# Kernel tuning notes

Hardware: AMD Instinct MI355X
Metric: run time of the kernel (lower is better)

Reference implementation:

```python
import jax, jax.numpy as jnp
import numpy as np

V, E, H, T = 30000, 512, 512, 32
B, L = 64, 512


def setup_inputs() -> dict:
    key = jax.random.key(0)
    ks = jax.random.split(key, 14)
    n = lambda k, shape: (jax.random.normal(k, shape, jnp.float32) * 0.05)
    return {
        "x": jax.random.randint(ks[0], (B, L), 0, V),
        "embedding": n(ks[1], (V, E)),
        # PyTorch LSTM params, gate order (i, f, g, o); biases b_ih+b_hh fused
        "w_ih_f": n(ks[2], (4 * H, E)),
        "w_hh_f": n(ks[3], (4 * H, H)),
        "b_f": n(ks[4], (4 * H,)),
        "w_ih_b": n(ks[5], (4 * H, E)),
        "w_hh_b": n(ks[6], (4 * H, H)),
        "b_b": n(ks[7], (4 * H,)),
        "W": n(ks[8], (T, 2 * H)),
        "b": n(ks[9], (T,)),
        # CRF params (torchcrf)
        "start": n(ks[10], (T,)),
        "end": n(ks[11], (T,)),
        "trans": n(ks[12], (T, T)),
    }


def _lstm(x, w_ih, w_hh, bias):
    # x: [L, B, E] -> hidden states [L, B, H]; PyTorch gate equations
    h_dim = w_hh.shape[1]
    xp = jnp.einsum('lbe,ge->lbg', x, w_ih) + bias  # precompute input proj [L,B,4H]

    def step(carry, xt):
        h, c = carry
        g = xt + h @ w_hh.T
        i, f, gg, o = jnp.split(g, 4, axis=-1)
        c = jax.nn.sigmoid(f) * c + jax.nn.sigmoid(i) * jnp.tanh(gg)
        h = jax.nn.sigmoid(o) * jnp.tanh(c)
        return (h, c), h

    bsz = x.shape[1]
    init = (jnp.zeros((bsz, h_dim), x.dtype), jnp.zeros((bsz, h_dim), x.dtype))
    _, hs = jax.lax.scan(step, init, xp)
    return hs


def _emissions(x, embedding, w_ih_f, w_hh_f, b_f, w_ih_b, w_hh_b, b_b, W, b):
    emb = embedding[x]                      # [B, L, E]
    xt = jnp.transpose(emb, (1, 0, 2))      # [L, B, E]
    hf = _lstm(xt, w_ih_f, w_hh_f, b_f)     # [L, B, H]
    hb = _lstm(xt[::-1], w_ih_b, w_hh_b, b_b)[::-1]
    h = jnp.concatenate([hf, hb], axis=-1)  # [L, B, 2H]
    return h @ W.T + b                      # [L, B, T]


def _viterbi(em, start, end, trans):
    # em: [L, B, T]; torchcrf CRF.decode with no mask (all timesteps valid)
    score = start + em[0]                   # [B, T]

    def step(score, em_t):
        nxt = score[:, :, None] + trans[None] + em_t[:, None, :]  # [B, T_prev, T_cur]
        return jnp.max(nxt, axis=1), jnp.argmax(nxt, axis=1)

    score, hist = jax.lax.scan(step, score, em[1:])  # hist: [L-1, B, T]
    score = score + end
    last = jnp.argmax(score, axis=-1)       # [B]

    def back(tag, idx_t):
        prev = jnp.take_along_axis(idx_t, tag[:, None], axis=1)[:, 0]
        return prev, prev

    _, prevs = jax.lax.scan(back, last, hist, reverse=True)  # [L-1, B]
    tags = jnp.concatenate([prevs, last[None]], axis=0)      # [L, B]
    return tags.T.astype(jnp.int32)                          # [B, L]


def reference(x, embedding, w_ih_f, w_hh_f, b_f, w_ih_b, w_hh_b, b_b, W, b, start, end, trans):
    em = _emissions(x, embedding, w_ih_f, w_hh_f, b_f, w_ih_b, w_hh_b, b_b, W, b)
    return _viterbi(em, start, end, trans)
```

## Files before the change

### kernel.cpp

```cpp
#include <hip/hip_runtime.h>
#include <cstdio>
#include <cstdint>


typedef float f32x4 __attribute__((ext_vector_type(4)));
typedef float f32x2 __attribute__((ext_vector_type(2)));
typedef short bf16x8 __attribute__((ext_vector_type(8)));
typedef unsigned short u16x4 __attribute__((ext_vector_type(4)));

#define PKFMA(ACC, W2, H2) \
    asm("v_pk_fma_f32 %0, %1, %2, %0" : "+v"(ACC) : "v"(W2), "v"(H2))

__device__ __forceinline__ unsigned short bf16_rne(float x) {
    unsigned u = __float_as_uint(x);
    return (unsigned short)((u + 0x7FFF + ((u >> 16) & 1)) >> 16);
}

__global__ __launch_bounds__(512) void k_gather(
    const int* __restrict__ x, const float* __restrict__ emb,
    unsigned short* __restrict__ egf)
{
    const int t   = blockIdx.x;
    const int tid = threadIdx.x;
    __shared__ int xv[64];
    if (tid < 64) xv[tid] = x[tid * 512 + t];
    __syncthreads();
    #pragma unroll
    for (int i = 0; i < 16; ++i) {
        const int unit = i * 512 + tid;
        const int b  = unit >> 7;
        const int k0 = (unit & 127) * 4;
        const float4 v = *reinterpret_cast<const float4*>(
            emb + (size_t)xv[b] * 512 + k0);
        const int ks   = k0 >> 6;
        const int kt   = (k0 >> 5) & 1;
        const int kk0  = k0 & 31;
        const int lgrp = (kk0 >> 2) & 3;
        const int rq   = kk0 >> 4;
        const int l    = lgrp * 16 + (b & 15);
        const int nt   = b >> 4;
        const size_t base =
            ((((((size_t)t * 8 + ks) * 2 + kt) * 4 + nt) * 2 + 0) * 64 + l) * 8 + rq * 4;
        const float xs[4] = {v.x, v.y, v.z, v.w};
        u16x4 hi, lo;
        #pragma unroll
        for (int j = 0; j < 4; ++j) {
            const unsigned short h = bf16_rne(xs[j]);
            hi[j] = h;
            const float hf = __uint_as_float(((unsigned)h) << 16);
            lo[j] = bf16_rne(xs[j] - hf);
        }
        *reinterpret_cast<u16x4*>(egf + base)       = hi;
        *reinterpret_cast<u16x4*>(egf + base + 512) = lo;
    }
}

__global__ __launch_bounds__(256) void k_pack(
    const float* __restrict__ wih_f, const float* __restrict__ whh_f,
    const float* __restrict__ wih_b, const float* __restrict__ whh_b,
    float* __restrict__ wpack)
{
    const int i = blockIdx.x * 256 + threadIdx.x;
    const int j   = i & 3;
    const int r   = (i >> 2) & 7;
    const int kc  = (i >> 5) & 15;
    const int sec = (i >> 9) & 1;
    const int ks  = (i >> 10) & 7;
    const int wg  = (i >> 13) & 255;
    const int dir = (i >> 21) & 1;
    const int k   = ks * 64 + kc * 4 + j;
    const int g   = r >> 1, colL = r & 1;
    const int rg  = g * 512 + wg * 2 + colL;
    const float* wih = dir ? wih_b : wih_f;
    const float* whh = dir ? whh_b : whh_f;
    const float v = sec ? whh[(size_t)rg * 512 + k] : wih[(size_t)rg * 512 + k];
    wpack[i] = v;
}

__global__ __launch_bounds__(256) void k_packA(
    const float* __restrict__ wih_f, const float* __restrict__ wih_b,
    unsigned short* __restrict__ afrag)
{
    const int idx = blockIdx.x * 256 + threadIdx.x;
    const int r   = idx & 7;
    const int l   = (idx >> 3) & 63;
    const int sel = (idx >> 9) & 1;
    const int kt  = (idx >> 10) & 1;
    const int ks  = (idx >> 11) & 7;
    const int wg  = (idx >> 14) & 255;
    const int dir = (idx >> 22) & 1;
    const int i   = l & 15;
    float w = 0.f;
    if (i < 8) {
        const int rg = (i >> 1) * 512 + wg * 2 + (i & 1);
        const int k  = ks * 64 + kt * 32 + (r >> 2) * 16 + ((l >> 4) & 3) * 4 + (r & 3);
        w = (dir ? wih_b : wih_f)[(size_t)rg * 512 + k];
    }
    const unsigned short hi = bf16_rne(w);
    unsigned short outv = hi;
    if (sel) {
        const float hf = __uint_as_float(((unsigned)hi) << 16);
        outv = bf16_rne(w - hf);
    }
    afrag[idx] = outv;
}

__global__ __launch_bounds__(512, 2) void k_lstm(
    const unsigned short* __restrict__ egf, const float* __restrict__ wpack,
    const unsigned short* __restrict__ afrag,
    const float* __restrict__ b_f, const float* __restrict__ b_b,
    float* __restrict__ h_f, float* __restrict__ h_b,
    int* __restrict__ bar)
{
    const int bid = blockIdx.x;
    const int dir = bid >> 8;
    const int wg  = bid & 255;
    float* HH       = dir ? h_b : h_f;
    const float* BS = dir ? b_b : b_f;
    int* ctr = bar + (size_t)dir * 65536;

    const int tid = threadIdx.x;
    const int b   = tid & 63;
    const int ks  = __builtin_amdgcn_readfirstlane(tid >> 6);

    __shared__ float wlds[8][512];
    __shared__ float partb[8 * 8 * 64];
    __shared__ float elds[2][8][8][64];
    __shared__ float hlds[64][2];

    {
        const float4* src = reinterpret_cast<const float4*>(
            wpack + (size_t)((dir * 256 + wg) * 8 + ks) * 1024 + 512);
        float4* dst = reinterpret_cast<float4*>(&wlds[ks][0]);
        #pragma unroll
        for (int i = 0; i < 2; ++i)
            dst[i * 64 + b] = src[i * 64 + b];
    }

    bf16x8 aHi[2], aLo[2];
    {
        const unsigned short* af = afrag
            + (size_t)((dir * 256 + wg) * 8 + ks) * 2048;
        #pragma unroll
        for (int kt = 0; kt < 2; ++kt) {
            aHi[kt] = *reinterpret_cast<const bf16x8*>(af + ((kt * 2 + 0) * 64 + b) * 8);
            aLo[kt] = *reinterpret_cast<const bf16x8*>(af + ((kt * 2 + 1) * 64 + b) * 8);
        }
    }

    const int colL = (tid >> 6) & 1;
    float bias4[4] = {0.f, 0.f, 0.f, 0.f};
    if (tid < 128) {
        #pragma unroll
        for (int g = 0; g < 4; ++g) bias4[g] = BS[g * 512 + wg * 2 + colL];
    }
    float cst = 0.f;

    {
        const int t0 = dir ? 511 : 0;
        const unsigned short* ef = egf + (size_t)t0 * 65536 + (size_t)ks * 8192;
        #pragma unroll
        for (int nt = 0; nt < 4; ++nt) {
            f32x4 d = {0.f, 0.f, 0.f, 0.f};
            #pragma unroll
            for (int kt = 0; kt < 2; ++kt) {
                const bf16x8 bh = *reinterpret_cast<const bf16x8*>(
                    ef + (((kt * 4 + nt) * 2 + 0) * 64 + b) * 8);
                const bf16x8 bl = *reinterpret_cast<const bf16x8*>(
                    ef + (((kt * 4 + nt) * 2 + 1) * 64 + b) * 8);
                d = __builtin_amdgcn_mfma_f32_16x16x32_bf16(aHi[kt], bh, d, 0, 0, 0);
                d = __builtin_amdgcn_mfma_f32_16x16x32_bf16(aHi[kt], bl, d, 0, 0, 0);
                d = __builtin_amdgcn_mfma_f32_16x16x32_bf16(aLo[kt], bh, d, 0, 0, 0);
            }
            const int i0 = (b >> 4) * 4;
            if (i0 < 8) {
                #pragma unroll
                for (int g = 0; g < 4; ++g)
                    elds[0][ks][i0 + g][nt * 16 + (b & 15)] = d[g];
            }
        }
    }
    __syncthreads();

    const float* wl = &wlds[ks][0];

    for (int s = 0; s < 512; ++s) {
        const int t = dir ? (511 - s) : s;
        f32x2 acc2[8];
        #pragma unroll
        for (int r = 0; r < 8; ++r) acc2[r] = (f32x2){0.f, 0.f};

        if (s > 0) {
            const int* fp = ctr + ((size_t)(s - 1) * 8 + ks) * 16;
            while (__hip_atomic_load(fp, __ATOMIC_RELAXED,
                                     __HIP_MEMORY_SCOPE_AGENT) < 32)
                __builtin_amdgcn_s_sleep(1);

            const int tp = dir ? (t + 1) : (t - 1);
            const f32x2* hq = reinterpret_cast<const f32x2*>(HH)
                              + ((size_t)tp * 256 + ks * 32) * 64 + b;
            #pragma unroll
            for (int half = 0; half < 2; ++half) {
                f32x2 hv[16];
                #pragma unroll
                for (int kq = 0; kq < 16; ++kq)
                    hv[kq] = hq[(size_t)(half * 16 + kq) * 64];
                #pragma unroll
                for (int kc = 0; kc < 8; ++kc) {
                    const float* wp = wl + (half * 8 + kc) * 32;
                    #pragma unroll
                    for (int r = 0; r < 8; ++r) {
                        const f32x4 w4 = *reinterpret_cast<const f32x4*>(wp + r * 4);
                        const f32x2 wlo = __builtin_shufflevector(w4, w4, 0, 1);
                        const f32x2 whi = __builtin_shufflevector(w4, w4, 2, 3);
                        PKFMA(acc2[r], wlo, hv[kc * 2]);
                        PKFMA(acc2[r], whi, hv[kc * 2 + 1]);
                    }
                }
            }
        }

        #pragma unroll
        for (int r = 0; r < 8; ++r)
            partb[(ks * 8 + r) * 64 + b] = acc2[r][0] + acc2[r][1];
        __syncthreads();

        if (tid < 128) {
            float g4[4];
            #pragma unroll
            for (int g = 0; g < 4; ++g) {
                const int r = g * 2 + colL;
                float v = bias4[g];
                #pragma unroll
                for (int w = 0; w < 8; ++w) v += partb[(w * 8 + r) * 64 + b];
                #pragma unroll
                for (int w = 0; w < 8; ++w) v += elds[s & 1][w][r][b];
                g4[g] = v;
            }
            const float si = 1.f / (1.f + expf(-g4[0]));
            const float sf = 1.f / (1.f + expf(-g4[1]));
            const float tg = tanhf(g4[2]);
            const float so = 1.f / (1.f + expf(-g4[3]));
            cst = sf * cst + si * tg;
            hlds[b][colL] = so * tanhf(cst);
        }
        __syncthreads();

        if (tid < 64) {
            f32x2 o;
            o[0] = hlds[tid][0]; o[1] = hlds[tid][1];
            float* dst = HH + (((size_t)t * 256 + wg) * 64 + tid) * 2;
            asm volatile("global_store_dwordx2 %0, %1, off sc1"
                         :: "v"(dst), "v"(o) : "memory");
            asm volatile("s_waitcnt vmcnt(0)" ::: "memory");
            if (tid == 0 && s < 511)
                __hip_atomic_fetch_add(
                    ctr + ((size_t)s * 8 + (wg >> 5)) * 16, 1,
                    __ATOMIC_RELAXED, __HIP_MEMORY_SCOPE_AGENT);
        }

        if (s < 511) {
            const int tn = dir ? (t - 1) : (t + 1);
            const unsigned short* ef = egf + (size_t)tn * 65536 + (size_t)ks * 8192;
            #pragma unroll
            for (int nt = 0; nt < 4; ++nt) {
                f32x4 d = {0.f, 0.f, 0.f, 0.f};
                #pragma unroll
                for (int kt = 0; kt < 2; ++kt) {
                    const bf16x8 bh = *reinterpret_cast<const bf16x8*>(
                        ef + (((kt * 4 + nt) * 2 + 0) * 64 + b) * 8);
                    const bf16x8 bl = *reinterpret_cast<const bf16x8*>(
                        ef + (((kt * 4 + nt) * 2 + 1) * 64 + b) * 8);
                    d = __builtin_amdgcn_mfma_f32_16x16x32_bf16(aHi[kt], bh, d, 0, 0, 0);
                    d = __builtin_amdgcn_mfma_f32_16x16x32_bf16(aHi[kt], bl, d, 0, 0, 0);
                    d = __builtin_amdgcn_mfma_f32_16x16x32_bf16(aLo[kt], bh, d, 0, 0, 0);
                }
                const int i0 = (b >> 4) * 4;
                if (i0 < 8) {
                    #pragma unroll
                    for (int g = 0; g < 4; ++g)
                        elds[(s + 1) & 1][ks][i0 + g][nt * 16 + (b & 15)] = d[g];
                }
            }
        }
    }
}

__global__ __launch_bounds__(256) void k_em(
    const float* __restrict__ hf, const float* __restrict__ hb,
    const float* __restrict__ Wm, const float* __restrict__ bias,
    float* __restrict__ em)
{
    const int t   = blockIdx.x;
    const int tid = threadIdx.x;
    const int b   = tid & 63;
    const int tg  = tid >> 6;
    __shared__ float Wl[128][33];
    float acc[8] = {};

    for (int ch = 0; ch < 8; ++ch) {
        {
            const int tag = tid >> 3;
            const int kq  = tid & 7;
            const float* src = Wm + (size_t)tag * 1024 + ch * 128 + kq * 16;
            #pragma unroll
            for (int ii = 0; ii < 4; ++ii) {
                const float4 v = *reinterpret_cast<const float4*>(src + ii * 4);
                const int k0 = kq * 16 + ii * 4;
                Wl[k0 + 0][tag] = v.x; Wl[k0 + 1][tag] = v.y;
                Wl[k0 + 2][tag] = v.z; Wl[k0 + 3][tag] = v.w;
            }
        }
        __syncthreads();
        const f32x2* hsrc2 = (ch < 4)
            ? (reinterpret_cast<const f32x2*>(hf) + ((size_t)t * 256 + ch * 64) * 64 + b)
            : (reinterpret_cast<const f32x2*>(hb) + ((size_t)t * 256 + (ch - 4) * 64) * 64 + b);
        #pragma unroll 4
        for (int c2l = 0; c2l < 64; ++c2l) {
            const f32x2 h2 = hsrc2[(size_t)c2l * 64];
            #pragma unroll
            for (int j = 0; j < 2; ++j)
                #pragma unroll
                for (int jt = 0; jt < 8; ++jt)
                    acc[jt] = fmaf(h2[j], Wl[c2l * 2 + j][tg * 8 + jt], acc[jt]);
        }
        __syncthreads();
    }

    #pragma unroll
    for (int jt = 0; jt < 8; ++jt) {
        const int tag = tg * 8 + jt;
        em[((size_t)t * 64 + b) * 32 + tag] = acc[jt] + bias[tag];
    }
}

__global__ __launch_bounds__(64) void k_vit(
    const float* __restrict__ em, const float* __restrict__ startv,
    const float* __restrict__ endv, const float* __restrict__ trans,
    int* __restrict__ out)
{
    const int b    = blockIdx.x;
    const int lane = threadIdx.x;
    const int c    = lane & 31;
    const bool act = lane < 32;
    __shared__ unsigned char hist[511][32];
    __shared__ int outb[512];

    float tr[32];
    #pragma unroll 8
    for (int p = 0; p < 32; ++p) tr[p] = trans[p * 32 + c];

    float s = act ? (startv[c] + em[(size_t)b * 32 + c]) : -1e30f;

    for (int t = 1; t < 512; ++t) {
        const float emc = act ? em[((size_t)t * 64 + b) * 32 + c] : 0.f;
        float m = -1e30f; int arg = 0;
        #pragma unroll 8
        for (int p = 0; p < 32; ++p) {
            const float v = __shfl(s, p) + tr[p] + emc;
            if (v > m) { m = v; arg = p; }
        }
        if (act) { s = m; hist[t - 1][c] = (unsigned char)arg; }
    }

    s = act ? (s + endv[c]) : -1e30f;
    int idx = act ? c : 63;
    #pragma unroll
    for (int off = 32; off >= 1; off >>= 1) {
        const float om = __shfl_down(s, off);
        const int   oi = __shfl_down(idx, off);
        if (om > s || (om == s && oi < idx)) { s = om; idx = oi; }
    }
    idx = __shfl(idx, 0);

    if (lane == 0) {
        int tag = idx;
        outb[511] = tag;
        for (int t = 510; t >= 0; --t) { tag = hist[t][tag]; outb[t] = tag; }
    }
    __syncthreads();
    for (int i = lane; i < 512; i += 64) out[(size_t)b * 512 + i] = outb[i];
}

extern "C" void kernel_launch(void* const* d_in, const int* in_sizes, int n_in,
                              void* d_out, int out_size, void* d_ws, size_t ws_size,
                              hipStream_t stream)
{
    const int*   x      = (const int*)d_in[0];
    const float* emb    = (const float*)d_in[1];
    const float* w_ih_f = (const float*)d_in[2];
    const float* w_hh_f = (const float*)d_in[3];
    const float* b_f    = (const float*)d_in[4];
    const float* w_ih_b = (const float*)d_in[5];
    const float* w_hh_b = (const float*)d_in[6];
    const float* b_b    = (const float*)d_in[7];
    const float* Wm     = (const float*)d_in[8];
    const float* bvec   = (const float*)d_in[9];
    const float* startv = (const float*)d_in[10];
    const float* endv   = (const float*)d_in[11];
    const float* trans  = (const float*)d_in[12];
    int* out = (int*)d_out;

    float* ws = (float*)d_ws;
    unsigned short* egf = (unsigned short*)ws;
    float* h_f   = ws + 16777216;
    float* h_b   = ws + 33554432;
    float* em    = ws + 50331648;
    float* wpack = ws + 51380224;
    unsigned short* afrag = (unsigned short*)(ws + 55574528);
    int*   bar   = (int*)(ws + 59768832);

    const size_t need = (size_t)(59768832 + 131072) * 4;
    if (ws_size < need) {
        fprintf(stderr, "kernel_launch: ws too small: %zu < %zu\n", ws_size, need);
        return;
    }

    (void)hipMemsetAsync(bar, 0, 524288, stream);
    k_gather<<<dim3(512),   512, 0, stream>>>(x, emb, egf);
    k_pack  <<<dim3(16384), 256, 0, stream>>>(w_ih_f, w_hh_f, w_ih_b, w_hh_b, wpack);
    k_packA <<<dim3(32768), 256, 0, stream>>>(w_ih_f, w_ih_b, afrag);
    k_lstm  <<<dim3(512),   512, 0, stream>>>(egf, wpack, afrag, b_f, b_b,
                                              h_f, h_b, bar);
    k_em    <<<dim3(512),   256, 0, stream>>>(h_f, h_b, Wm, bvec, em);
    k_vit   <<<dim3(64),     64, 0, stream>>>(em, startv, endv, trans, out);
}
```

Measured before the change: 7.014 ms.

## Replace atomic counter barrier with per-workgroup flags and prefetch input fragments

The cross-workgroup step barrier, a shared atomic counter per group of 32 workgroups, becomes one flag per workgroup per step. Each lane polls one flag, so the atomic-add contention goes away and waiters see only the producers they need. Input-projection B fragments for step s+1 are also loaded a step early into registers, so their global-load latency overlaps the current step's recurrence. This adds 64 registers per thread under a 512-thread, 2-block launch bound, which may cause spills, and doubles the barrier workspace.

After: 11.35 ms. 61.8% more time.

```diff
diff --git a/kernel.cpp b/kernel.cpp
--- a/kernel.cpp
+++ b/kernel.cpp
@@ -117,7 +117,7 @@
     const int wg  = bid & 255;
     float* HH       = dir ? h_b : h_f;
     const float* BS = dir ? b_b : b_f;
-    int* ctr = bar + (size_t)dir * 65536;
+    int* flg = bar + (size_t)dir * 131072;
 
     const int tid = threadIdx.x;
     const int b   = tid & 63;
@@ -156,6 +156,7 @@
     }
     float cst = 0.f;
 
+    bf16x8 bfh[2][4], bfl[2][4];
     {
         const int t0 = dir ? 511 : 0;
         const unsigned short* ef = egf + (size_t)t0 * 65536 + (size_t)ks * 8192;
@@ -179,6 +180,17 @@
                     elds[0][ks][i0 + g][nt * 16 + (b & 15)] = d[g];
             }
         }
+        const int t1 = dir ? 510 : 1;
+        const unsigned short* ef1 = egf + (size_t)t1 * 65536 + (size_t)ks * 8192;
+        #pragma unroll
+        for (int kt = 0; kt < 2; ++kt)
+            #pragma unroll
+            for (int nt = 0; nt < 4; ++nt) {
+                bfh[kt][nt] = *reinterpret_cast<const bf16x8*>(
+                    ef1 + (((kt * 4 + nt) * 2 + 0) * 64 + b) * 8);
+                bfl[kt][nt] = *reinterpret_cast<const bf16x8*>(
+                    ef1 + (((kt * 4 + nt) * 2 + 1) * 64 + b) * 8);
+            }
     }
     __syncthreads();
 
@@ -191,9 +203,9 @@
         for (int r = 0; r < 8; ++r) acc2[r] = (f32x2){0.f, 0.f};
 
         if (s > 0) {
-            const int* fp = ctr + ((size_t)(s - 1) * 8 + ks) * 16;
+            const int* fp = flg + (size_t)(s - 1) * 256 + ks * 32 + (b & 31);
             while (__hip_atomic_load(fp, __ATOMIC_RELAXED,
-                                     __HIP_MEMORY_SCOPE_AGENT) < 32)
+                                     __HIP_MEMORY_SCOPE_AGENT) == 0)
                 __builtin_amdgcn_s_sleep(1);
 
             const int tp = dir ? (t + 1) : (t - 1);
@@ -254,26 +266,19 @@
                          :: "v"(dst), "v"(o) : "memory");
             asm volatile("s_waitcnt vmcnt(0)" ::: "memory");
             if (tid == 0 && s < 511)
-                __hip_atomic_fetch_add(
-                    ctr + ((size_t)s * 8 + (wg >> 5)) * 16, 1,
-                    __ATOMIC_RELAXED, __HIP_MEMORY_SCOPE_AGENT);
+                __hip_atomic_store(flg + (size_t)s * 256 + wg, 1,
+                                   __ATOMIC_RELAXED, __HIP_MEMORY_SCOPE_AGENT);
         }
 
         if (s < 511) {
-            const int tn = dir ? (t - 1) : (t + 1);
-            const unsigned short* ef = egf + (size_t)tn * 65536 + (size_t)ks * 8192;
             #pragma unroll
             for (int nt = 0; nt < 4; ++nt) {
                 f32x4 d = {0.f, 0.f, 0.f, 0.f};
                 #pragma unroll
                 for (int kt = 0; kt < 2; ++kt) {
-                    const bf16x8 bh = *reinterpret_cast<const bf16x8*>(
-                        ef + (((kt * 4 + nt) * 2 + 0) * 64 + b) * 8);
-                    const bf16x8 bl = *reinterpret_cast<const bf16x8*>(
-                        ef + (((kt * 4 + nt) * 2 + 1) * 64 + b) * 8);
-                    d = __builtin_amdgcn_mfma_f32_16x16x32_bf16(aHi[kt], bh, d, 0, 0, 0);
-                    d = __builtin_amdgcn_mfma_f32_16x16x32_bf16(aHi[kt], bl, d, 0, 0, 0);
-                    d = __builtin_amdgcn_mfma_f32_16x16x32_bf16(aLo[kt], bh, d, 0, 0, 0);
+                    d = __builtin_amdgcn_mfma_f32_16x16x32_bf16(aHi[kt], bfh[kt][nt], d, 0, 0, 0);
+                    d = __builtin_amdgcn_mfma_f32_16x16x32_bf16(aHi[kt], bfl[kt][nt], d, 0, 0, 0);
+                    d = __builtin_amdgcn_mfma_f32_16x16x32_bf16(aLo[kt], bfh[kt][nt], d, 0, 0, 0);
                 }
                 const int i0 = (b >> 4) * 4;
                 if (i0 < 8) {
@@ -281,6 +286,19 @@
                     for (int g = 0; g < 4; ++g)
                         elds[(s + 1) & 1][ks][i0 + g][nt * 16 + (b & 15)] = d[g];
                 }
+            }
+            if (s < 510) {
+                const int tn2 = dir ? (509 - s) : (s + 2);
+                const unsigned short* ef = egf + (size_t)tn2 * 65536 + (size_t)ks * 8192;
+                #pragma unroll
+                for (int kt = 0; kt < 2; ++kt)
+                    #pragma unroll
+                    for (int nt = 0; nt < 4; ++nt) {
+                        bfh[kt][nt] = *reinterpret_cast<const bf16x8*>(
+                            ef + (((kt * 4 + nt) * 2 + 0) * 64 + b) * 8);
+                        bfl[kt][nt] = *reinterpret_cast<const bf16x8*>(
+                            ef + (((kt * 4 + nt) * 2 + 1) * 64 + b) * 8);
+                    }
             }
         }
     }
@@ -410,13 +428,13 @@
     unsigned short* afrag = (unsigned short*)(ws + 55574528);
     int*   bar   = (int*)(ws + 59768832);
 
-    const size_t need = (size_t)(59768832 + 131072) * 4;
+    const size_t need = (size_t)(59768832 + 262144) * 4;
     if (ws_size < need) {
         fprintf(stderr, "kernel_launch: ws too small: %zu < %zu\n", ws_size, need);
         return;
     }
 
-    (void)hipMemsetAsync(bar, 0, 524288, stream);
+    (void)hipMemsetAsync(bar, 0, 1048576, stream);
     k_gather<<<dim3(512),   512, 0, stream>>>(x, emb, egf);
     k_pack  <<<dim3(16384), 256, 0, stream>>>(w_ih_f, w_hh_f, w_ih_b, w_hh_b, wpack);
     k_packA <<<dim3(32768), 256, 0, stream>>>(w_ih_f, w_ih_b, afrag);
```
